# Optimization experiments

Hardware: AMD Instinct MI355X
Metric: run time of the kernel (lower is better)

Reference implementation:

```python
import jax, jax.numpy as jnp
import numpy as np

NUM_HEADS = 8
HEAD_DIM = 32  # in_channels // num_heads = 256 // 8


def setup_inputs() -> dict:
    key = jax.random.key(0)
    k1, k2, k3, k4 = jax.random.split(key, 4)
    B, C, H, W = 16, 256, 64, 64
    N = (H // 2) * (W // 2)  # 1024
    return {
        "x": jax.random.normal(k1, (B, C, H, W), dtype=jnp.float32),
        "w_qkv": jax.random.normal(k2, (3 * C, C), dtype=jnp.float32) * (1.0 / np.sqrt(C)),
        "b_qkv": jax.random.normal(k3, (3 * C,), dtype=jnp.float32) * 0.02,
        "pos_encoding": jax.random.normal(k4, (1, N, HEAD_DIM), dtype=jnp.float32) * 0.02,
    }


def reference(x, w_qkv, b_qkv, pos_encoding):
    B, C, H, W = x.shape
    Hp, Wp = H // 2, W // 2
    N = Hp * Wp
    # 1x1 conv: [B,C,H,W] -> [B,3C,H,W]
    y = jnp.einsum('bchw,oc->bohw', x, w_qkv) + b_qkv[None, :, None, None]
    # 2x2 max pool, stride 2
    y = y.reshape(B, 3 * C, Hp, 2, Wp, 2).max(axis=(3, 5))  # [B,3C,Hp,Wp]
    # split into q,k,v heads: channel order is (3, heads, head_dim)
    qkv = y.reshape(B, 3, NUM_HEADS, HEAD_DIM, N)
    qkv = qkv.transpose(1, 0, 2, 4, 3)  # [3,B,h,N,d]
    q, k, v = qkv[0], qkv[1], qkv[2]
    q = q + pos_encoding[:, None, :, :]  # broadcast over heads -> [B,h,N,d]
    scale = HEAD_DIM ** (-0.5)
    attn = jnp.einsum('bhnd,bhmd->bhnm', q, k) * scale
    attn = jax.nn.softmax(attn, axis=-1)
    out = jnp.einsum('bhnm,bhmd->bhnd', attn, v)  # [B,h,N,d]
    # transpose(2,3) then reshape -> [B, C, Hp, Wp]
    out = out.transpose(0, 1, 3, 2).reshape(B, C, Hp, Wp)
    return out
```

## Files before the change

kernel.cpp:

```cpp
#include <hip/hip_runtime.h>
#include <hip/hip_bf16.h>

typedef __bf16 bf16;
typedef bf16 bf16x8 __attribute__((ext_vector_type(8)));
typedef float f32x4 __attribute__((ext_vector_type(4)));
typedef float f32x16 __attribute__((ext_vector_type(16)));
typedef unsigned int u32;
typedef u32 u32x2 __attribute__((ext_vector_type(2)));
typedef u32 u32x4 __attribute__((ext_vector_type(4)));
typedef int i32x2 __attribute__((ext_vector_type(2)));


__device__ __forceinline__ u32 packbf2(float lo, float hi) {
    unsigned short a = __builtin_bit_cast(unsigned short, (bf16)lo);
    unsigned short b = __builtin_bit_cast(unsigned short, (bf16)hi);
    return (u32)a | ((u32)b << 16);
}

#if __has_builtin(__builtin_amdgcn_exp2f)
#define EXP2(x) __builtin_amdgcn_exp2f(x)
#else
#define EXP2(x) __expf((x)*0.69314718055994531f)
#endif

__device__ __forceinline__ i32x2 pl32swap(u32 a, u32 b) {
#if __has_builtin(__builtin_amdgcn_permlane32_swap)
    return __builtin_amdgcn_permlane32_swap((int)a, (int)b, false, false);
#else
    int lid = __builtin_amdgcn_mbcnt_hi(~0u, __builtin_amdgcn_mbcnt_lo(~0u, 0));
    u32 ax = (u32)__shfl_xor((int)a, 32);
    u32 bx = (u32)__shfl_xor((int)b, 32);
    i32x2 r;
    r.x = (int)(lid < 32 ? a : bx);
    r.y = (int)(lid < 32 ? ax : b);
    return r;
#endif
}

__device__ __forceinline__ f32x16 zero16() {
    f32x16 z;
#pragma unroll
    for (int i = 0; i < 16; ++i) z[i] = 0.f;
    return z;
}

__device__ __forceinline__ void gload_lds16(const bf16* gsrc, bf16* ldst) {
    __builtin_amdgcn_global_load_lds(
        (const __attribute__((address_space(1))) void*)gsrc,
        (__attribute__((address_space(3))) void*)ldst, 16, 0, 0);
}

#define MEMFENCE()                               \
    do {                                         \
        asm volatile("" ::: "memory");           \
        __builtin_amdgcn_sched_barrier(0);       \
    } while (0)

#define WAITV(N)                                                   \
    do {                                                           \
        asm volatile("s_waitcnt vmcnt(" #N ")" ::: "memory");      \
        __builtin_amdgcn_sched_barrier(0);                         \
    } while (0)

#define WAITLGKM()                                                 \
    do {                                                           \
        asm volatile("s_waitcnt lgkmcnt(0)" ::: "memory");         \
        __builtin_amdgcn_sched_barrier(0);                         \
    } while (0)

__global__ __launch_bounds__(256) void k_transpose_x(const float* __restrict__ x,
                                                     bf16* __restrict__ xt) {
    __shared__ __align__(16) bf16 tile[64][72];
    int b = blockIdx.z, cb = blockIdx.y, pb = blockIdx.x;
    int c0 = cb * 64, p0 = pb * 64;
    int t = threadIdx.x;
    int pr = (t & 15) * 4;
    int cr = t >> 4;
    const float* xp = x + ((size_t)(b * 256 + c0)) * 4096 + p0;
    for (int pass = 0; pass < 4; ++pass) {
        int c = cr + pass * 16;
        float4 v = *reinterpret_cast<const float4*>(xp + (size_t)c * 4096 + pr);
        tile[pr + 0][c] = (bf16)v.x;
        tile[pr + 1][c] = (bf16)v.y;
        tile[pr + 2][c] = (bf16)v.z;
        tile[pr + 3][c] = (bf16)v.w;
    }
    __syncthreads();
    bf16* op = xt + ((size_t)(b * 4096 + p0)) * 256 + c0;
    int c8 = (t & 7) * 8;
    int prow = t >> 3;
    for (int pass = 0; pass < 2; ++pass) {
        int p = prow + pass * 32;
        *reinterpret_cast<bf16x8*>(op + (size_t)p * 256 + c8) =
            *reinterpret_cast<const bf16x8*>(&tile[p][c8]);
    }
}

__global__ __launch_bounds__(256) void k_convert_w(const float* __restrict__ w,
                                                   bf16* __restrict__ wb) {
    int i = (blockIdx.x * 256 + threadIdx.x) * 8;
    float4 a = *reinterpret_cast<const float4*>(w + i);
    float4 b4 = *reinterpret_cast<const float4*>(w + i + 4);
    bf16x8 o;
    o[0] = (bf16)a.x;  o[1] = (bf16)a.y;  o[2] = (bf16)a.z;  o[3] = (bf16)a.w;
    o[4] = (bf16)b4.x; o[5] = (bf16)b4.y; o[6] = (bf16)b4.z; o[7] = (bf16)b4.w;
    *reinterpret_cast<bf16x8*>(wb + i) = o;
}

__global__ __launch_bounds__(256) void k_gemm_pool(const bf16* __restrict__ xt,
                                                   const bf16* __restrict__ wb,
                                                   const float* __restrict__ bias,
                                                   const float* __restrict__ pos,
                                                   bf16* __restrict__ Qb,
                                                   bf16* __restrict__ Kb,
                                                   bf16* __restrict__ Vb) {
    __shared__ __align__(16) bf16 bt[128 * 256];
    int b = blockIdx.y, nt = blockIdx.x;
    int p0 = nt * 128;
    int t = threadIdx.x;
    int w = t >> 6, lane = t & 63, g = lane >> 4, q = lane & 15;

    const bf16* xtp = xt + ((size_t)(b * 4096 + p0)) * 256;
    const bf16* wb_w = wb + (size_t)(w * 32) * 256;

    {
        int srow = t >> 5;
        int scb = t & 31;
        int wbase_row = w * 2;
#pragma unroll
        for (int pass = 0; pass < 16; ++pass) {
            int row = srow + pass * 8;
            int p = 2 * (row & 15) + ((row >> 4) & 1) + ((row >> 5) & 1) * 64 +
                    ((row >> 6) & 1) * 32;
            const bf16* gs = xtp + (size_t)p * 256 + ((scb ^ (row & 7)) << 3);
            gload_lds16(gs, bt + (pass * 8 + wbase_row) * 256);
        }
    }
    MEMFENCE();

    bf16x8 Ac[4], An[4];
#define LOADA(MT, KC, DST)                                                     \
    {                                                                          \
        _Pragma("unroll")                                                      \
        for (int ks = 0; ks < 2; ++ks)                                         \
            _Pragma("unroll")                                                  \
            for (int fr = 0; fr < 2; ++fr)                                     \
                DST[ks * 2 + fr] = *reinterpret_cast<const bf16x8*>(           \
                    wb_w + (size_t)((MT) * 128 + fr * 16 + q) * 256 +          \
                    (KC) * 64 + ks * 32 + g * 8);                              \
    }
    LOADA(0, 0, Ac);
    MEMFENCE();

    WAITV(4);
    __builtin_amdgcn_s_barrier();
    __builtin_amdgcn_sched_barrier(0);

    const float QSCALE = 0.2550406682649681f;

    for (int mt = 0; mt < 6; ++mt) {
        f32x4 acc[2][8];
#pragma unroll
        for (int fr = 0; fr < 2; ++fr)
#pragma unroll
            for (int fc = 0; fc < 8; ++fc) acc[fr][fc] = (f32x4){0.f, 0.f, 0.f, 0.f};

#pragma unroll
        for (int kc = 0; kc < 4; ++kc) {
            if (kc < 3) {
                LOADA(mt, kc + 1, An);
            } else if (mt < 5) {
                LOADA(mt + 1, 0, An);
            }
#pragma unroll
            for (int ks = 0; ks < 2; ++ks) {
#pragma unroll
                for (int fc = 0; fc < 8; ++fc) {
                    int co = kc * 64 + (((ks * 4 + g) ^ (q & 7)) << 3);
                    bf16x8 bfv = *reinterpret_cast<const bf16x8*>(
                        &bt[(fc * 16 + q) * 256 + co]);
                    acc[0][fc] = __builtin_amdgcn_mfma_f32_16x16x32_bf16(
                        Ac[ks * 2 + 0], bfv, acc[0][fc], 0, 0, 0);
                    acc[1][fc] = __builtin_amdgcn_mfma_f32_16x16x32_bf16(
                        Ac[ks * 2 + 1], bfv, acc[1][fc], 0, 0, 0);
                }
            }
#pragma unroll
            for (int i = 0; i < 4; ++i) Ac[i] = An[i];
        }

        int m0 = mt * 128;
        int sec = mt >> 1;
        int hh = ((m0 >> 5) + w) & 7;
        size_t bh = (size_t)(b * 8 + hh) * 32768;
#pragma unroll
        for (int fr = 0; fr < 2; ++fr) {
            int dbase = fr * 16 + g * 4;
            float4 bs = *reinterpret_cast<const float4*>(&bias[m0 + w * 32 + dbase]);
#pragma unroll
            for (int G = 0; G < 2; ++G) {
                int n_g = nt * 32 + G * 16 + q;
                float vm[4];
#pragma unroll
                for (int r = 0; r < 4; ++r) {
                    float a0 = fmaxf(acc[fr][4 * G + 0][r], acc[fr][4 * G + 1][r]);
                    float a1 = fmaxf(acc[fr][4 * G + 2][r], acc[fr][4 * G + 3][r]);
                    vm[r] = fmaxf(a0, a1) + ((const float*)&bs)[r];
                }
                if (sec == 0) {
                    float4 pv = *reinterpret_cast<const float4*>(
                        &pos[(size_t)n_g * 32 + dbase]);
                    u32x2 o2 = {packbf2((vm[0] + pv.x) * QSCALE, (vm[1] + pv.y) * QSCALE),
                                packbf2((vm[2] + pv.z) * QSCALE, (vm[3] + pv.w) * QSCALE)};
                    *reinterpret_cast<u32x2*>(Qb + bh + (size_t)n_g * 32 + dbase) = o2;
                } else if (sec == 1) {
                    u32x2 o2 = {packbf2(vm[0], vm[1]), packbf2(vm[2], vm[3])};
                    *reinterpret_cast<u32x2*>(Kb + bh + (size_t)n_g * 32 + dbase) = o2;
                } else {
#pragma unroll
                    for (int r = 0; r < 4; ++r)
                        Vb[bh + (size_t)(dbase + r) * 1024 + n_g] = (bf16)vm[r];
                }
            }
        }
    }
#undef LOADA
}

#define SUB2(K0, K1, V0, V1)                                                   \
    {                                                                          \
        f32x16 sa = __builtin_amdgcn_mfma_f32_32x32x16_bf16(K0, qfa0, zero16(), 0, 0, 0); \
        sa = __builtin_amdgcn_mfma_f32_32x32x16_bf16(K1, qfa1, sa, 0, 0, 0);   \
        f32x16 sb = __builtin_amdgcn_mfma_f32_32x32x16_bf16(K0, qfb0, zero16(), 0, 0, 0); \
        sb = __builtin_amdgcn_mfma_f32_32x32x16_bf16(K1, qfb1, sb, 0, 0, 0);   \
        float pa[16], pb[16];                                                  \
        _Pragma("unroll")                                                      \
        for (int r = 0; r < 16; ++r) pa[r] = EXP2(sa[r]);                      \
        _Pragma("unroll")                                                      \
        for (int r = 0; r < 16; ++r) pb[r] = EXP2(sb[r]);                      \
        run_a += (((pa[0]+pa[1])+(pa[2]+pa[3]))+((pa[4]+pa[5])+(pa[6]+pa[7]))) + \
                 (((pa[8]+pa[9])+(pa[10]+pa[11]))+((pa[12]+pa[13])+(pa[14]+pa[15]))); \
        run_b += (((pb[0]+pb[1])+(pb[2]+pb[3]))+((pb[4]+pb[5])+(pb[6]+pb[7]))) + \
                 (((pb[8]+pb[9])+(pb[10]+pb[11]))+((pb[12]+pb[13])+(pb[14]+pb[15]))); \
        {                                                                      \
            u32 k0 = packbf2(pa[0],pa[1]),   k1 = packbf2(pa[2],pa[3]);        \
            u32 k2 = packbf2(pa[4],pa[5]),   k3 = packbf2(pa[6],pa[7]);        \
            u32 k4 = packbf2(pa[8],pa[9]),   k5 = packbf2(pa[10],pa[11]);      \
            u32 k6 = packbf2(pa[12],pa[13]), k7 = packbf2(pa[14],pa[15]);      \
            i32x2 r02 = pl32swap(k0, k2); i32x2 r13 = pl32swap(k1, k3);        \
            i32x2 r46 = pl32swap(k4, k6); i32x2 r57 = pl32swap(k5, k7);        \
            u32x4 b0v = {(u32)r02.x, (u32)r13.x, (u32)r02.y, (u32)r13.y};      \
            u32x4 b1v = {(u32)r46.x, (u32)r57.x, (u32)r46.y, (u32)r57.y};      \
            bf16x8 pb0 = __builtin_bit_cast(bf16x8, b0v);                      \
            bf16x8 pb1 = __builtin_bit_cast(bf16x8, b1v);                      \
            oa = __builtin_amdgcn_mfma_f32_32x32x16_bf16(V0, pb0, oa, 0, 0, 0);\
            oa = __builtin_amdgcn_mfma_f32_32x32x16_bf16(V1, pb1, oa, 0, 0, 0);\
        }                                                                      \
        {                                                                      \
            u32 k0 = packbf2(pb[0],pb[1]),   k1 = packbf2(pb[2],pb[3]);        \
            u32 k2 = packbf2(pb[4],pb[5]),   k3 = packbf2(pb[6],pb[7]);        \
            u32 k4 = packbf2(pb[8],pb[9]),   k5 = packbf2(pb[10],pb[11]);      \
            u32 k6 = packbf2(pb[12],pb[13]), k7 = packbf2(pb[14],pb[15]);      \
            i32x2 r02 = pl32swap(k0, k2); i32x2 r13 = pl32swap(k1, k3);        \
            i32x2 r46 = pl32swap(k4, k6); i32x2 r57 = pl32swap(k5, k7);        \
            u32x4 b0v = {(u32)r02.x, (u32)r13.x, (u32)r02.y, (u32)r13.y};      \
            u32x4 b1v = {(u32)r46.x, (u32)r57.x, (u32)r46.y, (u32)r57.y};      \
            bf16x8 pb0 = __builtin_bit_cast(bf16x8, b0v);                      \
            bf16x8 pb1 = __builtin_bit_cast(bf16x8, b1v);                      \
            ob = __builtin_amdgcn_mfma_f32_32x32x16_bf16(V0, pb0, ob, 0, 0, 0);\
            ob = __builtin_amdgcn_mfma_f32_32x32x16_bf16(V1, pb1, ob, 0, 0, 0);\
        }                                                                      \
    }

__global__ __launch_bounds__(256) void k_attn(const bf16* __restrict__ Q,
                                              const bf16* __restrict__ K,
                                              const bf16* __restrict__ V,
                                              float* __restrict__ out) {
    __shared__ __align__(16) bf16 kt[2][2048];
    __shared__ __align__(16) bf16 vt[2][2048];
    int h = blockIdx.x, b = blockIdx.y, qb = blockIdx.z;
    int t = threadIdx.x, w = t >> 6, lane = t & 63;
    int lq = lane & 31, hi = lane >> 5, hi8 = hi * 8;
    size_t bh = (size_t)b * 8 + h;
    const bf16* Qp = Q + bh * 32768;
    const bf16* Kp = K + bh * 32768;
    const bf16* Vp = V + bh * 32768;
    float* Op = out + ((size_t)(b * 256 + h * 32)) * 1024;
    int q0 = qb * 256 + w * 32;

    bf16x8 qfa0 = *reinterpret_cast<const bf16x8*>(Qp + (size_t)(q0 + lq) * 32 + hi8);
    bf16x8 qfa1 = *reinterpret_cast<const bf16x8*>(Qp + (size_t)(q0 + lq) * 32 + 16 + hi8);
    bf16x8 qfb0 = *reinterpret_cast<const bf16x8*>(Qp + (size_t)(q0 + 128 + lq) * 32 + hi8);
    bf16x8 qfb1 = *reinterpret_cast<const bf16x8*>(Qp + (size_t)(q0 + 128 + lq) * 32 + 16 + hi8);

    int srow = lane & 31;
    int sh = w & 1, isV = w >> 1;
    const bf16* sg0;
    if (!isV) sg0 = Kp + (size_t)(sh * 32 + srow) * 32 + (lane >> 5) * 8;
    else      sg0 = Vp + (size_t)srow * 1024 + sh * 32 + (lane >> 5) * 8;
    const bf16* sg1 = sg0 + 16;
    int d0 = sh * 1024, d1 = sh * 1024 + 512;

#define STAGE64(BB, TT)                                                        \
    do {                                                                       \
        if (!isV) {                                                            \
            gload_lds16(sg0 + (size_t)(TT) * 2048, &kt[BB][d0]);               \
            gload_lds16(sg1 + (size_t)(TT) * 2048, &kt[BB][d1]);               \
        } else {                                                               \
            gload_lds16(sg0 + (TT) * 64, &vt[BB][d0]);                         \
            gload_lds16(sg1 + (TT) * 64, &vt[BB][d1]);                         \
        }                                                                      \
    } while (0)

    f32x16 oa = zero16(), ob = zero16();
    float run_a = 0.f, run_b = 0.f;

    STAGE64(0, 0);
    MEMFENCE();
    STAGE64(1, 1);
    MEMFENCE();

    for (int tt = 0; tt < 16; ++tt) {
        int cur = tt & 1;
        if (tt < 15) { WAITV(2); } else { WAITV(0); }
        __builtin_amdgcn_s_barrier();
        __builtin_amdgcn_sched_barrier(0);

        bf16x8 ka0 = *reinterpret_cast<const bf16x8*>(&kt[cur][hi * 256 + lq * 8]);
        bf16x8 ka1 = *reinterpret_cast<const bf16x8*>(&kt[cur][512 + hi * 256 + lq * 8]);
        bf16x8 va0 = *reinterpret_cast<const bf16x8*>(&vt[cur][hi * 256 + lq * 8]);
        bf16x8 va1 = *reinterpret_cast<const bf16x8*>(&vt[cur][512 + hi * 256 + lq * 8]);
        bf16x8 kb0 = *reinterpret_cast<const bf16x8*>(&kt[cur][1024 + hi * 256 + lq * 8]);
        bf16x8 kb1 = *reinterpret_cast<const bf16x8*>(&kt[cur][1536 + hi * 256 + lq * 8]);
        bf16x8 vb0 = *reinterpret_cast<const bf16x8*>(&vt[cur][1024 + hi * 256 + lq * 8]);
        bf16x8 vb1 = *reinterpret_cast<const bf16x8*>(&vt[cur][1536 + hi * 256 + lq * 8]);
        WAITLGKM();
        __builtin_amdgcn_s_barrier();
        __builtin_amdgcn_sched_barrier(0);
        if (tt < 14) STAGE64(cur, tt + 2);
        MEMFENCE();

        SUB2(ka0, ka1, va0, va1);
        SUB2(kb0, kb1, vb0, vb1);
    }
#undef STAGE64

    i32x2 rsa = pl32swap(__builtin_bit_cast(u32, run_a), __builtin_bit_cast(u32, run_a));
    float inva = 1.0f / (__builtin_bit_cast(float, (u32)rsa.x) +
                         __builtin_bit_cast(float, (u32)rsa.y));
    i32x2 rsb = pl32swap(__builtin_bit_cast(u32, run_b), __builtin_bit_cast(u32, run_b));
    float invb = 1.0f / (__builtin_bit_cast(float, (u32)rsb.x) +
                         __builtin_bit_cast(float, (u32)rsb.y));

#pragma unroll
    for (int r = 0; r < 16; ++r) {
        int dd = (r & 3) + 8 * (r >> 2) + 4 * hi;
        Op[(size_t)dd * 1024 + q0 + lq] = oa[r] * inva;
        Op[(size_t)dd * 1024 + q0 + 128 + lq] = ob[r] * invb;
    }
}

extern "C" void kernel_launch(void* const* d_in, const int* in_sizes, int n_in,
                              void* d_out, int out_size, void* d_ws, size_t ws_size,
                              hipStream_t stream) {
    const float* x = (const float*)d_in[0];
    const float* w = (const float*)d_in[1];
    const float* bias = (const float*)d_in[2];
    const float* pos = (const float*)d_in[3];
    float* outp = (float*)d_out;

    char* ws = (char*)d_ws;
    bf16* xt = (bf16*)(ws);
    bf16* wb = (bf16*)(ws + 33554432);
    bf16* Qb = (bf16*)(ws + 33947648);
    bf16* Kb = (bf16*)(ws + 42336256);
    bf16* Vb = (bf16*)(ws + 50724864);

    k_transpose_x<<<dim3(64, 4, 16), 256, 0, stream>>>(x, xt);
    k_convert_w<<<dim3(96), 256, 0, stream>>>(w, wb);
    k_gemm_pool<<<dim3(32, 16), 256, 0, stream>>>(xt, wb, bias, pos, Qb, Kb, Vb);
    k_attn<<<dim3(8, 16, 4), 256, 0, stream>>>(Qb, Kb, Vb, outp);
}
```

Before: 99.51 us.

## Halve per-block work in GEMM-pool and attention kernels to double grid size

The GEMM+maxpool kernel now processes 64 pixel rows (one 16-column pooled group) per block instead of 128, halving shared memory and accumulators and launching twice as many blocks with a 3-blocks-per-CU launch bound. The attention kernel now handles one 32-query tile per wave instead of two, doubling the grid along the query axis. The aim is more blocks and better occupancy across the CUs, at the cost of reloading the weight operands and K/V tiles more times in total.

```diff
diff --git a/kernel.cpp b/kernel.cpp
--- a/kernel.cpp
+++ b/kernel.cpp
@@ -107,20 +107,21 @@
     *reinterpret_cast<bf16x8*>(wb + i) = o;
 }
 
-__global__ __launch_bounds__(256) void k_gemm_pool(const bf16* __restrict__ xt,
-                                                   const bf16* __restrict__ wb,
-                                                   const float* __restrict__ bias,
-                                                   const float* __restrict__ pos,
-                                                   bf16* __restrict__ Qb,
-                                                   bf16* __restrict__ Kb,
-                                                   bf16* __restrict__ Vb) {
-    __shared__ __align__(16) bf16 bt[128 * 256];
+__global__ __launch_bounds__(256, 3) void k_gemm_pool(const bf16* __restrict__ xt,
+                                                      const bf16* __restrict__ wb,
+                                                      const float* __restrict__ bias,
+                                                      const float* __restrict__ pos,
+                                                      bf16* __restrict__ Qb,
+                                                      bf16* __restrict__ Kb,
+                                                      bf16* __restrict__ Vb) {
+    __shared__ __align__(16) bf16 bt[64 * 256];
     int b = blockIdx.y, nt = blockIdx.x;
-    int p0 = nt * 128;
+    int rr = nt >> 1, hh2 = nt & 1;
+    int base0 = rr * 128 + hh2 * 32;
     int t = threadIdx.x;
     int w = t >> 6, lane = t & 63, g = lane >> 4, q = lane & 15;
 
-    const bf16* xtp = xt + ((size_t)(b * 4096 + p0)) * 256;
+    const bf16* xtp = xt + (size_t)b * 4096 * 256;
     const bf16* wb_w = wb + (size_t)(w * 32) * 256;
 
     {
@@ -128,11 +129,12 @@
         int scb = t & 31;
         int wbase_row = w * 2;
 #pragma unroll
-        for (int pass = 0; pass < 16; ++pass) {
+        for (int pass = 0; pass < 8; ++pass) {
             int row = srow + pass * 8;
-            int p = 2 * (row & 15) + ((row >> 4) & 1) + ((row >> 5) & 1) * 64 +
-                    ((row >> 6) & 1) * 32;
-            const bf16* gs = xtp + (size_t)p * 256 + ((scb ^ (row & 7)) << 3);
+            int pl = 2 * (row & 15) + ((row >> 4) & 1);
+            int rowsel = (row >> 5) & 1;
+            size_t p = (size_t)(base0 + rowsel * 64 + pl);
+            const bf16* gs = xtp + p * 256 + ((scb ^ (row & 7)) << 3);
             gload_lds16(gs, bt + (pass * 8 + wbase_row) * 256);
         }
     }
@@ -157,13 +159,14 @@
     __builtin_amdgcn_sched_barrier(0);
 
     const float QSCALE = 0.2550406682649681f;
+    int n_g = rr * 32 + hh2 * 16 + q;
 
     for (int mt = 0; mt < 6; ++mt) {
-        f32x4 acc[2][8];
+        f32x4 acc[2][4];
 #pragma unroll
         for (int fr = 0; fr < 2; ++fr)
 #pragma unroll
-            for (int fc = 0; fc < 8; ++fc) acc[fr][fc] = (f32x4){0.f, 0.f, 0.f, 0.f};
+            for (int fc = 0; fc < 4; ++fc) acc[fr][fc] = (f32x4){0.f, 0.f, 0.f, 0.f};
 
 #pragma unroll
         for (int kc = 0; kc < 4; ++kc) {
@@ -175,7 +178,7 @@
 #pragma unroll
             for (int ks = 0; ks < 2; ++ks) {
 #pragma unroll
-                for (int fc = 0; fc < 8; ++fc) {
+                for (int fc = 0; fc < 4; ++fc) {
                     int co = kc * 64 + (((ks * 4 + g) ^ (q & 7)) << 3);
                     bf16x8 bfv = *reinterpret_cast<const bf16x8*>(
                         &bt[(fc * 16 + q) * 256 + co]);
@@ -197,79 +200,54 @@
         for (int fr = 0; fr < 2; ++fr) {
             int dbase = fr * 16 + g * 4;
             float4 bs = *reinterpret_cast<const float4*>(&bias[m0 + w * 32 + dbase]);
-#pragma unroll
-            for (int G = 0; G < 2; ++G) {
-                int n_g = nt * 32 + G * 16 + q;
-                float vm[4];
-#pragma unroll
-                for (int r = 0; r < 4; ++r) {
-                    float a0 = fmaxf(acc[fr][4 * G + 0][r], acc[fr][4 * G + 1][r]);
-                    float a1 = fmaxf(acc[fr][4 * G + 2][r], acc[fr][4 * G + 3][r]);
-                    vm[r] = fmaxf(a0, a1) + ((const float*)&bs)[r];
-                }
-                if (sec == 0) {
-                    float4 pv = *reinterpret_cast<const float4*>(
-                        &pos[(size_t)n_g * 32 + dbase]);
-                    u32x2 o2 = {packbf2((vm[0] + pv.x) * QSCALE, (vm[1] + pv.y) * QSCALE),
-                                packbf2((vm[2] + pv.z) * QSCALE, (vm[3] + pv.w) * QSCALE)};
-                    *reinterpret_cast<u32x2*>(Qb + bh + (size_t)n_g * 32 + dbase) = o2;
-                } else if (sec == 1) {
-                    u32x2 o2 = {packbf2(vm[0], vm[1]), packbf2(vm[2], vm[3])};
-                    *reinterpret_cast<u32x2*>(Kb + bh + (size_t)n_g * 32 + dbase) = o2;
-                } else {
-#pragma unroll
-                    for (int r = 0; r < 4; ++r)
-                        Vb[bh + (size_t)(dbase + r) * 1024 + n_g] = (bf16)vm[r];
-                }
+            float vm[4];
+#pragma unroll
+            for (int r = 0; r < 4; ++r) {
+                float a0 = fmaxf(acc[fr][0][r], acc[fr][1][r]);
+                float a1 = fmaxf(acc[fr][2][r], acc[fr][3][r]);
+                vm[r] = fmaxf(a0, a1) + ((const float*)&bs)[r];
+            }
+            if (sec == 0) {
+                float4 pv = *reinterpret_cast<const float4*>(
+                    &pos[(size_t)n_g * 32 + dbase]);
+                u32x2 o2 = {packbf2((vm[0] + pv.x) * QSCALE, (vm[1] + pv.y) * QSCALE),
+                            packbf2((vm[2] + pv.z) * QSCALE, (vm[3] + pv.w) * QSCALE)};
+                *reinterpret_cast<u32x2*>(Qb + bh + (size_t)n_g * 32 + dbase) = o2;
+            } else if (sec == 1) {
+                u32x2 o2 = {packbf2(vm[0], vm[1]), packbf2(vm[2], vm[3])};
+                *reinterpret_cast<u32x2*>(Kb + bh + (size_t)n_g * 32 + dbase) = o2;
+            } else {
+#pragma unroll
+                for (int r = 0; r < 4; ++r)
+                    Vb[bh + (size_t)(dbase + r) * 1024 + n_g] = (bf16)vm[r];
             }
         }
     }
 #undef LOADA
 }
 
-#define SUB2(K0, K1, V0, V1)                                                   \
+#define SUBTILE_FULL(K0, K1, V0, V1)                                           \
     {                                                                          \
-        f32x16 sa = __builtin_amdgcn_mfma_f32_32x32x16_bf16(K0, qfa0, zero16(), 0, 0, 0); \
-        sa = __builtin_amdgcn_mfma_f32_32x32x16_bf16(K1, qfa1, sa, 0, 0, 0);   \
-        f32x16 sb = __builtin_amdgcn_mfma_f32_32x32x16_bf16(K0, qfb0, zero16(), 0, 0, 0); \
-        sb = __builtin_amdgcn_mfma_f32_32x32x16_bf16(K1, qfb1, sb, 0, 0, 0);   \
-        float pa[16], pb[16];                                                  \
+        f32x16 s = __builtin_amdgcn_mfma_f32_32x32x16_bf16(K0, qf0, zero16(), 0, 0, 0); \
+        s = __builtin_amdgcn_mfma_f32_32x32x16_bf16(K1, qf1, s, 0, 0, 0);      \
+        float p[16];                                                           \
         _Pragma("unroll")                                                      \
-        for (int r = 0; r < 16; ++r) pa[r] = EXP2(sa[r]);                      \
-        _Pragma("unroll")                                                      \
-        for (int r = 0; r < 16; ++r) pb[r] = EXP2(sb[r]);                      \
-        run_a += (((pa[0]+pa[1])+(pa[2]+pa[3]))+((pa[4]+pa[5])+(pa[6]+pa[7]))) + \
-                 (((pa[8]+pa[9])+(pa[10]+pa[11]))+((pa[12]+pa[13])+(pa[14]+pa[15]))); \
-        run_b += (((pb[0]+pb[1])+(pb[2]+pb[3]))+((pb[4]+pb[5])+(pb[6]+pb[7]))) + \
-                 (((pb[8]+pb[9])+(pb[10]+pb[11]))+((pb[12]+pb[13])+(pb[14]+pb[15]))); \
-        {                                                                      \
-            u32 k0 = packbf2(pa[0],pa[1]),   k1 = packbf2(pa[2],pa[3]);        \
-            u32 k2 = packbf2(pa[4],pa[5]),   k3 = packbf2(pa[6],pa[7]);        \
-            u32 k4 = packbf2(pa[8],pa[9]),   k5 = packbf2(pa[10],pa[11]);      \
-            u32 k6 = packbf2(pa[12],pa[13]), k7 = packbf2(pa[14],pa[15]);      \
-            i32x2 r02 = pl32swap(k0, k2); i32x2 r13 = pl32swap(k1, k3);        \
-            i32x2 r46 = pl32swap(k4, k6); i32x2 r57 = pl32swap(k5, k7);        \
-            u32x4 b0v = {(u32)r02.x, (u32)r13.x, (u32)r02.y, (u32)r13.y};      \
-            u32x4 b1v = {(u32)r46.x, (u32)r57.x, (u32)r46.y, (u32)r57.y};      \
-            bf16x8 pb0 = __builtin_bit_cast(bf16x8, b0v);                      \
-            bf16x8 pb1 = __builtin_bit_cast(bf16x8, b1v);                      \
-            oa = __builtin_amdgcn_mfma_f32_32x32x16_bf16(V0, pb0, oa, 0, 0, 0);\
-            oa = __builtin_amdgcn_mfma_f32_32x32x16_bf16(V1, pb1, oa, 0, 0, 0);\
-        }                                                                      \
-        {                                                                      \
-            u32 k0 = packbf2(pb[0],pb[1]),   k1 = packbf2(pb[2],pb[3]);        \
-            u32 k2 = packbf2(pb[4],pb[5]),   k3 = packbf2(pb[6],pb[7]);        \
-            u32 k4 = packbf2(pb[8],pb[9]),   k5 = packbf2(pb[10],pb[11]);      \
-            u32 k6 = packbf2(pb[12],pb[13]), k7 = packbf2(pb[14],pb[15]);      \
-            i32x2 r02 = pl32swap(k0, k2); i32x2 r13 = pl32swap(k1, k3);        \
-            i32x2 r46 = pl32swap(k4, k6); i32x2 r57 = pl32swap(k5, k7);        \
-            u32x4 b0v = {(u32)r02.x, (u32)r13.x, (u32)r02.y, (u32)r13.y};      \
-            u32x4 b1v = {(u32)r46.x, (u32)r57.x, (u32)r46.y, (u32)r57.y};      \
-            bf16x8 pb0 = __builtin_bit_cast(bf16x8, b0v);                      \
-            bf16x8 pb1 = __builtin_bit_cast(bf16x8, b1v);                      \
-            ob = __builtin_amdgcn_mfma_f32_32x32x16_bf16(V0, pb0, ob, 0, 0, 0);\
-            ob = __builtin_amdgcn_mfma_f32_32x32x16_bf16(V1, pb1, ob, 0, 0, 0);\
-        }                                                                      \
+        for (int r = 0; r < 16; ++r) p[r] = EXP2(s[r]);                        \
+        float ts = (((p[0]+p[1])+(p[2]+p[3]))+((p[4]+p[5])+(p[6]+p[7]))) +     \
+                   (((p[8]+p[9])+(p[10]+p[11]))+((p[12]+p[13])+(p[14]+p[15])));\
+        run_s += ts;                                                           \
+        u32 pk0 = packbf2(p[0],p[1]),   pk1 = packbf2(p[2],p[3]);              \
+        u32 pk2 = packbf2(p[4],p[5]),   pk3 = packbf2(p[6],p[7]);              \
+        u32 pk4 = packbf2(p[8],p[9]),   pk5 = packbf2(p[10],p[11]);            \
+        u32 pk6 = packbf2(p[12],p[13]), pk7 = packbf2(p[14],p[15]);            \
+        i32x2 r02 = pl32swap(pk0, pk2); i32x2 r13 = pl32swap(pk1, pk3);        \
+        i32x2 r46 = pl32swap(pk4, pk6); i32x2 r57 = pl32swap(pk5, pk7);        \
+        u32x4 b0v = {(u32)r02.x, (u32)r13.x, (u32)r02.y, (u32)r13.y};          \
+        u32x4 b1v = {(u32)r46.x, (u32)r57.x, (u32)r46.y, (u32)r57.y};          \
+        bf16x8 pb0 = __builtin_bit_cast(bf16x8, b0v);                          \
+        bf16x8 pb1 = __builtin_bit_cast(bf16x8, b1v);                          \
+        o = __builtin_amdgcn_mfma_f32_32x32x16_bf16(V0, pb0, o, 0, 0, 0);      \
+        o = __builtin_amdgcn_mfma_f32_32x32x16_bf16(V1, pb1, o, 0, 0, 0);      \
     }
 
 __global__ __launch_bounds__(256) void k_attn(const bf16* __restrict__ Q,
@@ -286,12 +264,10 @@
     const bf16* Kp = K + bh * 32768;
     const bf16* Vp = V + bh * 32768;
     float* Op = out + ((size_t)(b * 256 + h * 32)) * 1024;
-    int q0 = qb * 256 + w * 32;
-
-    bf16x8 qfa0 = *reinterpret_cast<const bf16x8*>(Qp + (size_t)(q0 + lq) * 32 + hi8);
-    bf16x8 qfa1 = *reinterpret_cast<const bf16x8*>(Qp + (size_t)(q0 + lq) * 32 + 16 + hi8);
-    bf16x8 qfb0 = *reinterpret_cast<const bf16x8*>(Qp + (size_t)(q0 + 128 + lq) * 32 + hi8);
-    bf16x8 qfb1 = *reinterpret_cast<const bf16x8*>(Qp + (size_t)(q0 + 128 + lq) * 32 + 16 + hi8);
+    int q0 = qb * 128 + w * 32;
+
+    bf16x8 qf0 = *reinterpret_cast<const bf16x8*>(Qp + (size_t)(q0 + lq) * 32 + hi8);
+    bf16x8 qf1 = *reinterpret_cast<const bf16x8*>(Qp + (size_t)(q0 + lq) * 32 + 16 + hi8);
 
     int srow = lane & 31;
     int sh = w & 1, isV = w >> 1;
@@ -312,8 +288,8 @@
         }                                                                      \
     } while (0)
 
-    f32x16 oa = zero16(), ob = zero16();
-    float run_a = 0.f, run_b = 0.f;
+    f32x16 o = zero16();
+    float run_s = 0.f;
 
     STAGE64(0, 0);
     MEMFENCE();
@@ -340,23 +316,19 @@
         if (tt < 14) STAGE64(cur, tt + 2);
         MEMFENCE();
 
-        SUB2(ka0, ka1, va0, va1);
-        SUB2(kb0, kb1, vb0, vb1);
+        SUBTILE_FULL(ka0, ka1, va0, va1);
+        SUBTILE_FULL(kb0, kb1, vb0, vb1);
     }
 #undef STAGE64
 
-    i32x2 rsa = pl32swap(__builtin_bit_cast(u32, run_a), __builtin_bit_cast(u32, run_a));
-    float inva = 1.0f / (__builtin_bit_cast(float, (u32)rsa.x) +
-                         __builtin_bit_cast(float, (u32)rsa.y));
-    i32x2 rsb = pl32swap(__builtin_bit_cast(u32, run_b), __builtin_bit_cast(u32, run_b));
-    float invb = 1.0f / (__builtin_bit_cast(float, (u32)rsb.x) +
-                         __builtin_bit_cast(float, (u32)rsb.y));
+    i32x2 rs = pl32swap(__builtin_bit_cast(u32, run_s), __builtin_bit_cast(u32, run_s));
+    float tot = __builtin_bit_cast(float, (u32)rs.x) + __builtin_bit_cast(float, (u32)rs.y);
+    float inv = 1.0f / tot;
 
 #pragma unroll
     for (int r = 0; r < 16; ++r) {
         int dd = (r & 3) + 8 * (r >> 2) + 4 * hi;
-        Op[(size_t)dd * 1024 + q0 + lq] = oa[r] * inva;
-        Op[(size_t)dd * 1024 + q0 + 128 + lq] = ob[r] * invb;
+        Op[(size_t)dd * 1024 + q0 + lq] = o[r] * inv;
     }
 }
 
@@ -378,6 +350,6 @@
 
     k_transpose_x<<<dim3(64, 4, 16), 256, 0, stream>>>(x, xt);
     k_convert_w<<<dim3(96), 256, 0, stream>>>(w, wb);
-    k_gemm_pool<<<dim3(32, 16), 256, 0, stream>>>(xt, wb, bias, pos, Qb, Kb, Vb);
-    k_attn<<<dim3(8, 16, 4), 256, 0, stream>>>(Qb, Kb, Vb, outp);
-}
+    k_gemm_pool<<<dim3(64, 16), 256, 0, stream>>>(xt, wb, bias, pos, Qb, Kb, Vb);
+    k_attn<<<dim3(8, 16, 8), 256, 0, stream>>>(Qb, Kb, Vb, outp);
+}
```

Result: slower. 189.0 us (+89.9%).
